# Kernel optimization log

Measured on AMD Instinct MI355X. Metric: run time of the kernel, lower is better.

Reference implementation:

```python
import jax, jax.numpy as jnp
import numpy as np

N, H, B, D, O = 512, 40, 8, 384, 62
DT = 1e-4  # step_size
BOUND = 500.0  # coupling saturation bound
# Jansen-Rit constants (ParamsJR defaults, all variances 0 -> non-learnable)
A_, a_, B_, b_, g_ = 3.25, 100.0, 22.0, 50.0, 100.0
c1, c2, c3, c4 = 135.0, 135.0 * 0.8, 135.0 * 0.25, 135.0 * 0.25
STD_IN, VMAX, V0, R_, MU, K_, KI = 100.0, 5.0, 6.0, 0.56, 0.5, 5.0, 1.0


def setup_inputs() -> dict:
    key = jax.random.key(0)
    ks = jax.random.split(key, 9)
    return {
        "input": jax.random.normal(ks[0], (N, H, B), jnp.float32),
        "noise_in": jax.random.normal(ks[1], (N, H, B, 1), jnp.float32),
        "noise_out": jax.random.normal(ks[2], (N, B), jnp.float32),
        "hx": jax.random.uniform(ks[3], (N, 6), jnp.float32),
        "hE": jax.random.normal(ks[4], (N, D), jnp.float32),
        "w_bb": jax.random.normal(ks[5], (N, N), jnp.float32),
        "sc": jax.random.uniform(ks[6], (N, N), jnp.float32),
        "lm": jax.random.normal(ks[7], (O, N), jnp.float32),
        "delays": jax.random.randint(ks[8], (N, N), 0, D, jnp.int32),
    }


def _sigmoid(x):
    # potential-to-rate operator
    return VMAX / (1.0 + jnp.exp(R_ * (V0 - x)))


def _sys2nd(Aamp, a, u, x, v):
    return Aamp * a * u - 2.0 * a * v - a * a * x


def reference(input, noise_in, noise_out, hx, hE, w_bb, sc, lm, delays):
    # normalized symmetric coupling matrix
    w = jnp.exp(w_bb) * sc
    ws = jnp.log1p(0.5 * (w + w.T))
    w_n = ws / jnp.linalg.norm(ws)            # Frobenius norm, as torch.linalg.norm
    rowsum = jnp.sum(w_n, axis=1)[:, None]    # dg = -diag(rowsum); dg @ x == -rowsum*x

    M, E, I = hx[:, 0:1], hx[:, 1:2], hx[:, 2:3]
    Mv, Ev, Iv = hx[:, 3:4], hx[:, 4:5], hx[:, 5:6]

    def hidden_step(carry, inp):
        M, E, I, Mv, Ev, Iv, hE = carry
        u, nz = inp  # [N,1] each
        Ed = jnp.take_along_axis(hE, delays, axis=1)      # Ed[i,j] = hE[i, delays[i,j]]
        LEd = jnp.sum(w_n * Ed.T, axis=1, keepdims=True)  # [N,1]
        noiseE = nz * STD_IN
        stim = K_ * KI * u
        rM = _sigmoid(E - I)
        rE = c2 * _sigmoid(c1 * M)
        rI = c4 * _sigmoid(c3 * M)
        coupled = g_ * (LEd - rowsum * (E - I))
        coupling = BOUND * jnp.tanh(coupled / BOUND)
        Mn = M + DT * Mv
        En = E + DT * Ev
        In = I + DT * Iv
        Mvn = Mv + DT * _sys2nd(A_, a_, rM, M, Mv)
        Evn = Ev + DT * _sys2nd(A_, a_, rE + coupling + stim + noiseE + MU, E, Ev)
        Ivn = Iv + DT * _sys2nd(B_, b_, rI, I, Iv)
        hE = hE.at[:, 0].set(En[:, 0] - In[:, 0])  # in-place slot-0 write, as in torch
        return (Mn, En, In, Mvn, Evn, Ivn, hE), None

    def batch_step(state, inp):
        u_seq, nz_seq = inp  # [H,N,1]
        state, _ = jax.lax.scan(hidden_step, state, (u_seq, nz_seq))
        M, E, I, Mv, Ev, Iv, hE = state
        hE = jnp.concatenate([E - I, hE[:, :-1]], axis=1)  # shift delay buffer
        eeg = 0.0005 * (lm @ (E - I))  # [O,1]
        return (M, E, I, Mv, Ev, Iv, hE), (M, E, I, Mv, Ev, Iv, eeg)

    u_all = jnp.transpose(input, (2, 1, 0))[..., None]            # [B,H,N,1]
    nz_all = jnp.transpose(noise_in[..., 0], (2, 1, 0))[..., None]
    state0 = (M, E, I, Mv, Ev, Iv, hE)
    state, outs = jax.lax.scan(batch_step, state0, (u_all, nz_all))
    Ms, Es, Is, Mvs, Evs, Ivs, eegs = outs  # [B,N,1] each, eeg [B,O,1]

    stack = lambda x: x[..., 0].T  # -> [N,B] (or [O,B]), matches torch.cat(axis=1)
    Mf, Ef, If, Mvf, Evf, Ivf, hEf = state
    current_state = jnp.concatenate([Mf, Ef, If, Mvf, Evf, Ivf], axis=1)  # [N,6]
    return (current_state, stack(eegs), stack(Es), stack(Is), stack(Ms),
            stack(Evs), stack(Ivs), stack(Mvs), hEf)
```

## Files before the change

kernel.cpp:

```cpp
#include <hip/hip_runtime.h>
#include <math.h>

#define N_    512
#define H_    40
#define B_N   8
#define D_    384
#define O_    62
#define RW    392
#define SMAX  13
#define CMAX  28

#define OUT_STATE 0
#define OUT_EEG   3072
#define OUT_ES    3568
#define OUT_IS    7664
#define OUT_MS    11760
#define OUT_EVS   15856
#define OUT_IVS   19952
#define OUT_MVS   24048
#define OUT_HE    28144

#define SIGK      0.8079092228978195f
#define SIGC      4.847455337386917f
#define SIGK_E    109.06774509120563f
#define SIGK_I    27.266936272801407f
#define TANHS     0.5770780163555854f

#define BARRIER() asm volatile("s_waitcnt lgkmcnt(0)\n\ts_barrier" ::: "memory")

__global__ void k_cnt(const int* __restrict__ delays, int* __restrict__ s0c) {
    int i = blockIdx.x, t = threadIdx.x;
    bool f1 = (delays[t * N_ + i] == 0);
    bool f2 = (delays[(t + 256) * N_ + i] == 0);
    unsigned long long m1 = __ballot(f1), m2 = __ballot(f2);
    __shared__ int pc[4];
    int wave = t >> 6, lane = t & 63;
    if (lane == 0) pc[wave] = __popcll(m1) + __popcll(m2);
    __syncthreads();
    if (t == 0) {
        int s = pc[0] + pc[1] + pc[2] + pc[3];
        s0c[i] = (s > SMAX) ? SMAX : s;
    }
}

__global__ void __launch_bounds__(512)
k_perm(const int* __restrict__ s0c, int* __restrict__ perm,
       int* __restrict__ invp, int* __restrict__ wmaxc) {
    int t = threadIdx.x;
    int wave = t >> 6, lane = t & 63;
    int cnt = s0c[t];
    __shared__ int wc[14 * 8];
    __shared__ int base[14 * 8];
    unsigned long long below = (lane == 0) ? 0ull : ((~0ull) >> (64 - lane));
    for (int c = 0; c < 14; c++) {
        unsigned long long m = __ballot(cnt == c);
        if (lane == 0) wc[c * 8 + wave] = __popcll(m);
    }
    __syncthreads();
    if (t == 0) {
        int s = 0;
        for (int c = 0; c < 14; c++)
            for (int w = 0; w < 8; w++) { base[c * 8 + w] = s; s += wc[c * 8 + w]; }
    }
    __syncthreads();
    int pos = 0;
    for (int c = 0; c < 14; c++) {
        unsigned long long m = __ballot(cnt == c);
        if (cnt == c) pos = base[c * 8 + wave] + __popcll(m & below);
    }
    perm[pos] = t;
    invp[t] = pos;
    if ((pos & 63) == 63) wmaxc[pos >> 6] = cnt;
}

__global__ void k_prep(const float* __restrict__ wbb, const float* __restrict__ sc,
                       const float* __restrict__ hE_in, const int* __restrict__ delays,
                       const int* __restrict__ invp,
                       float* __restrict__ ws, float* __restrict__ ring,
                       float* __restrict__ rowsumP, float* __restrict__ sumsq,
                       float* __restrict__ s0w, int* __restrict__ s0j,
                       float* __restrict__ s1w, int* __restrict__ s1p) {
    int i = blockIdx.x;
    int t = threadIdx.x;
    int ip = invp[i];
    __shared__ float wsrow[N_];
    __shared__ float red[256];
    __shared__ int cnt_c[8];
    __shared__ int bases[8];
    __shared__ int runbase;

    if (t < SMAX) { s0j[t * N_ + ip] = i;        s0w[t * N_ + ip] = 0.f; }
    if (t < CMAX) { s1p[t * N_ + ip] = (1 << 9); s1w[t * N_ + ip] = 0.f; }
    if (t < 9)    { ring[i * RW + t] = 0.f; }

    float ssq = 0.f, rsum = 0.f;
    for (int j = t; j < N_; j += 256) {
        float w = 0.5f * (expf(wbb[i * N_ + j]) * sc[i * N_ + j] +
                          expf(wbb[j * N_ + i]) * sc[j * N_ + i]);
        float v = log1pf(w);
        ws[i * N_ + j] = v;
        wsrow[j] = v;
        ssq += v * v;
        rsum += v;
    }
    for (int k = t; k < D_ - 1; k += 256) ring[i * RW + 9 + k] = hE_in[i * D_ + 1 + k];

    red[t] = ssq; __syncthreads();
    for (int s = 128; s > 0; s >>= 1) { if (t < s) red[t] += red[t + s]; __syncthreads(); }
    if (t == 0) sumsq[i] = red[0];
    __syncthreads();
    red[t] = rsum; __syncthreads();
    for (int s = 128; s > 0; s >>= 1) { if (t < s) red[t] += red[t + s]; __syncthreads(); }
    if (t == 0) rowsumP[ip] = red[0];
    __syncthreads();

    int wave = t >> 6, lane = t & 63;
    int dv1 = delays[t * N_ + i];
    int dv2 = delays[(t + 256) * N_ + i];
    unsigned long long below = (lane == 0) ? 0ull : ((~0ull) >> (64 - lane));
    for (int d = 0; d < 8; d++) {
        bool f1 = (dv1 == d), f2 = (dv2 == d);
        unsigned long long m1 = __ballot(f1);
        unsigned long long m2 = __ballot(f2);
        if (lane == 0) { cnt_c[wave] = __popcll(m1); cnt_c[wave + 4] = __popcll(m2); }
        __syncthreads();
        if (t == 0) {
            int s = (d == 0) ? 0 : runbase;
            for (int c = 0; c < 8; c++) { bases[c] = s; s += cnt_c[c]; }
            if (d == 0) runbase = 0;
            else runbase = s;
        }
        __syncthreads();
        if (d == 0) {
            if (f1) { int pos = bases[wave]     + __popcll(m1 & below);
                      if (pos < SMAX) { s0j[pos * N_ + ip] = t;       s0w[pos * N_ + ip] = wsrow[t]; } }
            if (f2) { int pos = bases[wave + 4] + __popcll(m2 & below);
                      if (pos < SMAX) { s0j[pos * N_ + ip] = t + 256; s0w[pos * N_ + ip] = wsrow[t + 256]; } }
        } else {
            if (f1) { int pos = bases[wave]     + __popcll(m1 & below);
                      if (pos < CMAX) { s1p[pos * N_ + ip] = t | (d << 9);         s1w[pos * N_ + ip] = wsrow[t]; } }
            if (f2) { int pos = bases[wave + 4] + __popcll(m2 & below);
                      if (pos < CMAX) { s1p[pos * N_ + ip] = (t + 256) | (d << 9); s1w[pos * N_ + ip] = wsrow[t + 256]; } }
        }
    }
}

__global__ void __launch_bounds__(512)
k_hist(const float* __restrict__ ws, const int* __restrict__ delays,
       const float* __restrict__ ring, const int* __restrict__ invp,
       const float* __restrict__ input, const float* __restrict__ noise_in,
       float* __restrict__ drv, float* __restrict__ bp8) {
    if (blockIdx.x < H_ * B_N) {
        int bb = blockIdx.x & 7, h = blockIdx.x >> 3;
        int dst = (bb * H_ + h) * N_;
        int nn = threadIdx.x;
        float u  = input[nn * (H_ * B_N) + h * B_N + bb];
        float nz = noise_in[nn * (H_ * B_N) + h * B_N + bb];
        drv[dst + invp[nn]] = fmaf(0.1625f, u, fmaf(3.25f, nz, 16.26625f));
    }
    int b  = blockIdx.x >> 6;
    int ib = (blockIdx.x >> 3) & 7;
    int jb = blockIdx.x & 7;
    int wave = threadIdx.x >> 6, lane = threadIdx.x & 63;
    int i = ib * 64 + lane;
    int off = 8 - b;
    float acc = 0.f;
    int j0 = jb * 64 + wave * 8;
#pragma unroll
    for (int jj = 0; jj < 8; jj++) {
        int j = j0 + jj;
        int d = delays[j * N_ + i];
        float w = ws[j * N_ + i];
        float v = ring[j * RW + off + d];
        acc += (d > 0 ? w : 0.f) * v;
    }
    __shared__ float part[8][64];
    part[wave][lane] = acc; __syncthreads();
    if (wave == 0) {
        float s = 0.f;
#pragma unroll
        for (int w2 = 0; w2 < 8; w2++) s += part[w2][lane];
        bp8[(b * 8 + jb) * N_ + invp[i]] = s;
    }
}

#define LOADK0(K) int jb_##K = s0j[K * N_ + t] << 2; float w_##K = s0w[K * N_ + t] * scale;
#define G(CB, K)  (*(const float*)((const char*)(CB) + jb_##K))

#define PRF(CB)                                                                \
    if (wmax > 0) { g0 = G(CB,0); g1 = G(CB,1); }                              \
    if (wmax > 2) { g2 = G(CB,2); g3 = G(CB,3); }                              \
    if (wmax > 4) { g4 = G(CB,4); g5 = G(CB,5); g6 = G(CB,6); g7 = G(CB,7);    \
                    g8 = G(CB,8); g9 = G(CB,9); g10 = G(CB,10);                \
                    g11 = G(CB,11); g12 = G(CB,12); }

#define STEP(CB, CN)                                                           \
  {                                                                            \
    float d_n = *dnext; dnext += N_;                                           \
    float En = fmaf(1e-4f, Ev, E);                                             \
    float In = fmaf(1e-4f, Iv, I);                                             \
    float Mn = fmaf(1e-4f, Mv, M);                                             \
    (CN)[n] = En - In;                                                         \
    float ei = E - I;                                                          \
    float rMr = __builtin_amdgcn_rcpf(1.0f + __builtin_amdgcn_exp2f(fmaf(-SIGK,   ei, SIGC))); \
    float rEr = __builtin_amdgcn_rcpf(1.0f + __builtin_amdgcn_exp2f(fmaf(-SIGK_E, M,  SIGC))); \
    float rIr = __builtin_amdgcn_rcpf(1.0f + __builtin_amdgcn_exp2f(fmaf(-SIGK_I, M,  SIGC))); \
    float Mvn = fmaf(0.1625f,  rMr, fmaf(0.98f, Mv, -M));                      \
    float Ivn = fmaf(18.5625f, rIr, fmaf(0.99f, Iv, -0.25f * I));              \
    float pre = fmaf(17.55f,   rEr, fmaf(0.98f, Ev, -E) + d_c);                \
    float a0 = 0.f, a1 = 0.f;                                                  \
    if (wmax > 0) { a0 = w_0 * g0; a1 = w_1 * g1; }                            \
    if (wmax > 2) { a0 = fmaf(w_2, g2, a0); a1 = fmaf(w_3, g3, a1); }          \
    if (wmax > 4) { a0 = fmaf(w_4,  g4,  a0); a1 = fmaf(w_5,  g5,  a1);        \
                    a0 = fmaf(w_6,  g6,  a0); a1 = fmaf(w_7,  g7,  a1);        \
                    a0 = fmaf(w_8,  g8,  a0); a1 = fmaf(w_9,  g9,  a1);        \
                    a0 = fmaf(w_10, g10, a0); a1 = fmaf(w_11, g11, a1);        \
                    a0 = fmaf(w_12, g12, a0); }                                \
    float arg = fmaf(-rs, ei, base) + (a0 + a1);                               \
    float cr = __builtin_amdgcn_rcpf(1.0f + __builtin_amdgcn_exp2f(arg));      \
    float Evn = fmaf(-32.5f, cr, pre);                                         \
    M = Mn; E = En; I = In; Mv = Mvn; Ev = Evn; Iv = Iv + 0.f; Iv = Ivn;       \
    d_c = d_n;                                                                 \
    BARRIER();                                                                 \
    PRF(CN)                                                                    \
  }

__global__ void __launch_bounds__(512)
k_hidden(const float* __restrict__ drv, const float* __restrict__ hE_in,
         const float* __restrict__ hx, const float* __restrict__ bp8,
         const float* __restrict__ sumsq, const float* __restrict__ rowsumP,
         const float* __restrict__ s0w, const int* __restrict__ s0j,
         const float* __restrict__ s1w, const int* __restrict__ s1p,
         const int* __restrict__ perm, const int* __restrict__ wmaxc,
         float* __restrict__ ring, float* __restrict__ fing,
         float* __restrict__ out) {
    __shared__ float curr0[N_];
    __shared__ float curr1[N_];
    __shared__ float fin_l[B_N * N_];
    __shared__ float red[N_];
    int t = threadIdx.x;
    int n = perm[t];
    int wmax = __builtin_amdgcn_readfirstlane(wmaxc[t >> 6]);

    red[t] = sumsq[t];
    __syncthreads();
    if (t < 64) {
        float s2 = 0.f;
#pragma unroll
        for (int q = 0; q < 8; q++) s2 += red[t + 64 * q];
#pragma unroll
        for (int off = 32; off > 0; off >>= 1) s2 += __shfl_xor(s2, off, 64);
        if (t == 0) red[0] = s2;
    }
    __syncthreads();
    float scale = TANHS / sqrtf(red[0]);

    LOADK0(0)  LOADK0(1)  LOADK0(2)  LOADK0(3)  LOADK0(4)  LOADK0(5)  LOADK0(6)
    LOADK0(7)  LOADK0(8)  LOADK0(9)  LOADK0(10) LOADK0(11) LOADK0(12)
    int   s1p_r[CMAX];
    float s1w_r[CMAX];
#pragma unroll
    for (int k = 0; k < CMAX; k++) { s1p_r[k] = s1p[k * N_ + t]; s1w_r[k] = s1w[k * N_ + t] * scale; }

    float M  = hx[n * 6 + 0], E  = hx[n * 6 + 1], I  = hx[n * 6 + 2];
    float Mv = hx[n * 6 + 3], Ev = hx[n * 6 + 4], Iv = hx[n * 6 + 5];
    float rs = rowsumP[t] * scale;

    float hp[8];
#pragma unroll
    for (int k = 0; k < 8; k++) hp[k] = bp8[k * N_ + t];

    const float* dnext = drv + t + N_;
    float d_c = drv[t];

    float g0=0.f,g1=0.f,g2=0.f,g3=0.f,g4=0.f,g5=0.f,g6=0.f,g7=0.f,g8=0.f,
          g9=0.f,g10=0.f,g11=0.f,g12=0.f;

#pragma unroll
    for (int k = 0; k < B_N; k++) fin_l[k * N_ + t] = 0.f;
    curr0[n] = hE_in[n * D_];
    __syncthreads();
    PRF(curr0)

    for (int b = 0; b < B_N; b++) {
        float hist = (((hp[0] + hp[1]) + (hp[2] + hp[3])) +
                      ((hp[4] + hp[5]) + (hp[6] + hp[7]))) * scale;
        float corr = 0.f;
#pragma unroll
        for (int k = 0; k < CMAX; k++) {
            int p = s1p_r[k];
            int off = (((b + 8 - (p >> 9)) & 7) << 11) + ((p & 511) << 2);
            corr = fmaf(s1w_r[k], *(const float*)((const char*)fin_l + off), corr);
        }
        float base = hist + corr;

        int bn = (b < B_N - 1) ? b + 1 : b;
#pragma unroll
        for (int k = 0; k < 8; k++) hp[k] = bp8[(bn * 8 + k) * N_ + t];

        for (int hh = 0; hh < H_ / 2; hh++) {
            STEP(curr0, curr1)
            STEP(curr1, curr0)
        }
        float eif = E - I;
        fin_l[b * N_ + n] = eif;
        out[OUT_ES  + n * B_N + b] = E;
        out[OUT_IS  + n * B_N + b] = I;
        out[OUT_MS  + n * B_N + b] = M;
        out[OUT_EVS + n * B_N + b] = Ev;
        out[OUT_IVS + n * B_N + b] = Iv;
        out[OUT_MVS + n * B_N + b] = Mv;
        ring[n * RW + (7 - b)] = eif;
        ring[n * RW + (8 - b)] = eif;
        fing[b * N_ + n] = eif;
        BARRIER();
    }

    out[n * 6 + 0] = M;  out[n * 6 + 1] = E;  out[n * 6 + 2] = I;
    out[n * 6 + 3] = Mv; out[n * 6 + 4] = Ev; out[n * 6 + 5] = Iv;
}

__global__ void k_post(const float* __restrict__ ring, const float* __restrict__ fing,
                       const float* __restrict__ lm, float* __restrict__ out) {
    int bi = blockIdx.x;
    int lane = threadIdx.x;
    if (bi < N_) {
#pragma unroll
        for (int q = 0; q < 6; q++) {
            int k = lane + 64 * q;
            if (k < D_) out[OUT_HE + bi * D_ + k] = ring[bi * RW + k];
        }
    } else {
        int o = bi - N_;
        float lv[8];
#pragma unroll
        for (int q = 0; q < 8; q++) lv[q] = lm[o * N_ + 64 * q + lane];
        for (int b = 0; b < B_N; b++) {
            float p = 0.f;
#pragma unroll
            for (int q = 0; q < 8; q++) p = fmaf(lv[q], fing[b * N_ + 64 * q + lane], p);
#pragma unroll
            for (int off = 32; off > 0; off >>= 1) p += __shfl_down(p, off, 64);
            if (lane == 0) out[OUT_EEG + o * B_N + b] = 0.0005f * p;
        }
    }
}

extern "C" void kernel_launch(void* const* d_in, const int* in_sizes, int n_in,
                              void* d_out, int out_size, void* d_ws, size_t ws_size,
                              hipStream_t stream) {
    const float* input    = (const float*)d_in[0];
    const float* noise_in = (const float*)d_in[1];
    const float* hx       = (const float*)d_in[3];
    const float* hE       = (const float*)d_in[4];
    const float* wbb      = (const float*)d_in[5];
    const float* sc       = (const float*)d_in[6];
    const float* lm       = (const float*)d_in[7];
    const int*   delays   = (const int*)d_in[8];
    float* out = (float*)d_out;

    float* F    = (float*)d_ws;
    float* drv  = F;
    float* wsm  = drv + 164352;
    float* ring = wsm + 262144;
    float* bp8  = ring + 200704;
    float* rswP = bp8 + 32768;
    float* ssq  = rswP + 512;
    float* s0w  = ssq + 512;
    int*   s0j  = (int*)(s0w + N_ * SMAX);
    float* s1w  = (float*)(s0j + N_ * SMAX);
    int*   s1p  = (int*)(s1w + N_ * CMAX);
    float* fing = (float*)(s1p + N_ * CMAX);
    int*   s0c  = (int*)(fing + B_N * N_);
    int*   perm = s0c + N_;
    int*   invp = perm + N_;
    int*   wmaxc = invp + N_;

    k_cnt<<<N_, 256, 0, stream>>>(delays, s0c);
    k_perm<<<1, N_, 0, stream>>>(s0c, perm, invp, wmaxc);
    k_prep<<<N_, 256, 0, stream>>>(wbb, sc, hE, delays, invp,
                                   wsm, ring, rswP, ssq, s0w, s0j, s1w, s1p);
    k_hist<<<512, 512, 0, stream>>>(wsm, delays, ring, invp, input, noise_in, drv, bp8);
    k_hidden<<<1, N_, 0, stream>>>(drv, hE, hx, bp8, ssq, rswP,
                                   s0w, s0j, s1w, s1p, perm, wmaxc, ring, fing, out);
    k_post<<<N_ + O_, 64, 0, stream>>>(ring, fing, lm, out);
}
```

Before: 142.1 us.

## Halve barriers by computing two hidden steps per sync with four-slot buffer

The hidden-state loop now advances two Euler steps between each barrier. It relies on the next-next E-I value being computable locally, and it uses a four-slot shared buffer so that gathers for two steps can be prefetched together. The drive array is transposed per node so each thread loads four consecutive steps as a float4. The E-rate sigmoid now reuses the I-rate exponential through a fourth-power identity, and the prep kernel uses fast exp/log intrinsics. The goal is to halve barrier count and cut transcendental work, at the cost of higher register use and small numeric differences.

```diff
diff --git a/kernel.cpp b/kernel.cpp
--- a/kernel.cpp
+++ b/kernel.cpp
@@ -9,6 +9,7 @@
 #define RW    392
 #define SMAX  13
 #define CMAX  28
+#define DRVS  336
 
 #define OUT_STATE 0
 #define OUT_EEG   3072
@@ -25,6 +26,7 @@
 #define SIGK_E    109.06774509120563f
 #define SIGK_I    27.266936272801407f
 #define TANHS     0.5770780163555854f
+#define C3Q       4.190944e-05f
 
 #define BARRIER() asm volatile("s_waitcnt lgkmcnt(0)\n\ts_barrier" ::: "memory")
 
@@ -95,9 +97,9 @@
 
     float ssq = 0.f, rsum = 0.f;
     for (int j = t; j < N_; j += 256) {
-        float w = 0.5f * (expf(wbb[i * N_ + j]) * sc[i * N_ + j] +
-                          expf(wbb[j * N_ + i]) * sc[j * N_ + i]);
-        float v = log1pf(w);
+        float w = 0.5f * (__expf(wbb[i * N_ + j]) * sc[i * N_ + j] +
+                          __expf(wbb[j * N_ + i]) * sc[j * N_ + i]);
+        float v = 0.6931471805599453f * __builtin_amdgcn_logf(1.0f + w);
         ws[i * N_ + j] = v;
         wsrow[j] = v;
         ssq += v * v;
@@ -152,11 +154,11 @@
        float* __restrict__ drv, float* __restrict__ bp8) {
     if (blockIdx.x < H_ * B_N) {
         int bb = blockIdx.x & 7, h = blockIdx.x >> 3;
-        int dst = (bb * H_ + h) * N_;
+        int step = bb * H_ + h;
         int nn = threadIdx.x;
         float u  = input[nn * (H_ * B_N) + h * B_N + bb];
         float nz = noise_in[nn * (H_ * B_N) + h * B_N + bb];
-        drv[dst + invp[nn]] = fmaf(0.1625f, u, fmaf(3.25f, nz, 16.26625f));
+        drv[(size_t)invp[nn] * DRVS + step] = fmaf(0.1625f, u, fmaf(3.25f, nz, 16.26625f));
     }
     int b  = blockIdx.x >> 6;
     int ib = (blockIdx.x >> 3) & 7;
@@ -185,45 +187,56 @@
 }
 
 #define LOADK0(K) int jb_##K = s0j[K * N_ + t] << 2; float w_##K = s0w[K * N_ + t] * scale;
-#define G(CB, K)  (*(const float*)((const char*)(CB) + jb_##K))
-
-#define PRF(CB)                                                                \
-    if (wmax > 0) { g0 = G(CB,0); g1 = G(CB,1); }                              \
-    if (wmax > 2) { g2 = G(CB,2); g3 = G(CB,3); }                              \
-    if (wmax > 4) { g4 = G(CB,4); g5 = G(CB,5); g6 = G(CB,6); g7 = G(CB,7);    \
-                    g8 = G(CB,8); g9 = G(CB,9); g10 = G(CB,10);                \
-                    g11 = G(CB,11); g12 = G(CB,12); }
-
-#define STEP(CB, CN)                                                           \
+#define GS(SLOT, K) (*(const float*)((const char*)curr4 + ((SLOT) << 11) + jb_##K))
+
+#define PRFS(S, SLOT)                                                          \
+    if (wmax > 0) { g##S##0 = GS(SLOT,0); g##S##1 = GS(SLOT,1); }              \
+    if (wmax > 2) { g##S##2 = GS(SLOT,2); g##S##3 = GS(SLOT,3); }              \
+    if (wmax > 4) { g##S##4 = GS(SLOT,4); g##S##5 = GS(SLOT,5);                \
+                    g##S##6 = GS(SLOT,6); g##S##7 = GS(SLOT,7);                \
+                    g##S##8 = GS(SLOT,8); g##S##9 = GS(SLOT,9);                \
+                    g##S##10 = GS(SLOT,10); g##S##11 = GS(SLOT,11);            \
+                    g##S##12 = GS(SLOT,12); }
+
+#define STEPCORE(DV, S, WSLOT)                                                 \
   {                                                                            \
-    float d_n = *dnext; dnext += N_;                                           \
+    float e0 = __builtin_amdgcn_exp2f(fmaf(-SIGK, ei_c, SIGC));                \
+    float uu = __builtin_amdgcn_exp2f(fmaf(-SIGK_I, M, SIGC));                 \
+    float u2 = uu * uu;                                                        \
+    float u4 = u2 * u2;                                                        \
+    float rMr = __builtin_amdgcn_rcpf(1.0f + e0);                              \
+    float rIr = __builtin_amdgcn_rcpf(1.0f + uu);                              \
+    float rEr = __builtin_amdgcn_rcpf(fmaf(C3Q, u4, 1.0f));                    \
     float En = fmaf(1e-4f, Ev, E);                                             \
     float In = fmaf(1e-4f, Iv, I);                                             \
     float Mn = fmaf(1e-4f, Mv, M);                                             \
-    (CN)[n] = En - In;                                                         \
-    float ei = E - I;                                                          \
-    float rMr = __builtin_amdgcn_rcpf(1.0f + __builtin_amdgcn_exp2f(fmaf(-SIGK,   ei, SIGC))); \
-    float rEr = __builtin_amdgcn_rcpf(1.0f + __builtin_amdgcn_exp2f(fmaf(-SIGK_E, M,  SIGC))); \
-    float rIr = __builtin_amdgcn_rcpf(1.0f + __builtin_amdgcn_exp2f(fmaf(-SIGK_I, M,  SIGC))); \
+    float a0 = 0.f, a1 = 0.f;                                                  \
+    if (wmax > 0) { a0 = w_0 * g##S##0; a1 = w_1 * g##S##1; }                  \
+    if (wmax > 2) { a0 = fmaf(w_2, g##S##2, a0); a1 = fmaf(w_3, g##S##3, a1); }\
+    if (wmax > 4) { a0 = fmaf(w_4,  g##S##4,  a0); a1 = fmaf(w_5,  g##S##5,  a1);\
+                    a0 = fmaf(w_6,  g##S##6,  a0); a1 = fmaf(w_7,  g##S##7,  a1);\
+                    a0 = fmaf(w_8,  g##S##8,  a0); a1 = fmaf(w_9,  g##S##9,  a1);\
+                    a0 = fmaf(w_10, g##S##10, a0); a1 = fmaf(w_11, g##S##11, a1);\
+                    a0 = fmaf(w_12, g##S##12, a0); }                           \
+    float arg = fmaf(-rs, ei_c, base) + (a0 + a1);                             \
+    float e1 = __builtin_amdgcn_exp2f(arg);                                    \
+    float cr = __builtin_amdgcn_rcpf(1.0f + e1);                               \
     float Mvn = fmaf(0.1625f,  rMr, fmaf(0.98f, Mv, -M));                      \
     float Ivn = fmaf(18.5625f, rIr, fmaf(0.99f, Iv, -0.25f * I));              \
-    float pre = fmaf(17.55f,   rEr, fmaf(0.98f, Ev, -E) + d_c);                \
-    float a0 = 0.f, a1 = 0.f;                                                  \
-    if (wmax > 0) { a0 = w_0 * g0; a1 = w_1 * g1; }                            \
-    if (wmax > 2) { a0 = fmaf(w_2, g2, a0); a1 = fmaf(w_3, g3, a1); }          \
-    if (wmax > 4) { a0 = fmaf(w_4,  g4,  a0); a1 = fmaf(w_5,  g5,  a1);        \
-                    a0 = fmaf(w_6,  g6,  a0); a1 = fmaf(w_7,  g7,  a1);        \
-                    a0 = fmaf(w_8,  g8,  a0); a1 = fmaf(w_9,  g9,  a1);        \
-                    a0 = fmaf(w_10, g10, a0); a1 = fmaf(w_11, g11, a1);        \
-                    a0 = fmaf(w_12, g12, a0); }                                \
-    float arg = fmaf(-rs, ei, base) + (a0 + a1);                               \
-    float cr = __builtin_amdgcn_rcpf(1.0f + __builtin_amdgcn_exp2f(arg));      \
-    float Evn = fmaf(-32.5f, cr, pre);                                         \
-    M = Mn; E = En; I = In; Mv = Mvn; Ev = Evn; Iv = Iv + 0.f; Iv = Ivn;       \
-    d_c = d_n;                                                                 \
-    BARRIER();                                                                 \
-    PRF(CN)                                                                    \
+    float Evn = fmaf(-32.5f, cr, fmaf(17.55f, rEr, fmaf(0.98f, Ev, -E) + (DV)));\
+    float En2 = fmaf(1e-4f, Evn, En);                                          \
+    float In2 = fmaf(1e-4f, Ivn, In);                                          \
+    curr4[WSLOT][n] = En2 - In2;                                               \
+    M = Mn; E = En; I = In; Mv = Mvn; Ev = Evn; Iv = Ivn;                      \
+    ei_c = En - In;                                                            \
   }
+
+#define BLOCK(S0, S1, W0, W1, DVA, DVB)                                        \
+    PRFS(A, S0)                                                                \
+    PRFS(B, S1)                                                                \
+    STEPCORE(DVA, A, W0)                                                       \
+    STEPCORE(DVB, B, W1)                                                       \
+    BARRIER();
 
 __global__ void __launch_bounds__(512)
 k_hidden(const float* __restrict__ drv, const float* __restrict__ hE_in,
@@ -234,8 +247,7 @@
          const int* __restrict__ perm, const int* __restrict__ wmaxc,
          float* __restrict__ ring, float* __restrict__ fing,
          float* __restrict__ out) {
-    __shared__ float curr0[N_];
-    __shared__ float curr1[N_];
+    __shared__ float curr4[4][N_];
     __shared__ float fin_l[B_N * N_];
     __shared__ float red[N_];
     int t = threadIdx.x;
@@ -270,17 +282,17 @@
 #pragma unroll
     for (int k = 0; k < 8; k++) hp[k] = bp8[k * N_ + t];
 
-    const float* dnext = drv + t + N_;
-    float d_c = drv[t];
-
-    float g0=0.f,g1=0.f,g2=0.f,g3=0.f,g4=0.f,g5=0.f,g6=0.f,g7=0.f,g8=0.f,
-          g9=0.f,g10=0.f,g11=0.f,g12=0.f;
-
+    float gA0=0.f,gA1=0.f,gA2=0.f,gA3=0.f,gA4=0.f,gA5=0.f,gA6=0.f,gA7=0.f,
+          gA8=0.f,gA9=0.f,gA10=0.f,gA11=0.f,gA12=0.f;
+    float gB0=0.f,gB1=0.f,gB2=0.f,gB3=0.f,gB4=0.f,gB5=0.f,gB6=0.f,gB7=0.f,
+          gB8=0.f,gB9=0.f,gB10=0.f,gB11=0.f,gB12=0.f;
+
+    float ei_c = E - I;
 #pragma unroll
     for (int k = 0; k < B_N; k++) fin_l[k * N_ + t] = 0.f;
-    curr0[n] = hE_in[n * D_];
-    __syncthreads();
-    PRF(curr0)
+    curr4[0][n] = hE_in[n * D_];
+    curr4[1][n] = fmaf(1e-4f, Ev, E) - fmaf(1e-4f, Iv, I);
+    __syncthreads();
 
     for (int b = 0; b < B_N; b++) {
         float hist = (((hp[0] + hp[1]) + (hp[2] + hp[3])) +
@@ -298,11 +310,16 @@
 #pragma unroll
         for (int k = 0; k < 8; k++) hp[k] = bp8[(bn * 8 + k) * N_ + t];
 
-        for (int hh = 0; hh < H_ / 2; hh++) {
-            STEP(curr0, curr1)
-            STEP(curr1, curr0)
-        }
-        float eif = E - I;
+        const float4* sp4 = (const float4*)(drv + (size_t)t * DRVS + b * H_);
+        float4 dc = sp4[0];
+        for (int q = 0; q < 10; q++) {
+            float4 dn = sp4[q + 1];
+            BLOCK(0, 1, 2, 3, dc.x, dc.y)
+            BLOCK(2, 3, 0, 1, dc.z, dc.w)
+            dc = dn;
+        }
+
+        float eif = ei_c;
         fin_l[b * N_ + n] = eif;
         out[OUT_ES  + n * B_N + b] = E;
         out[OUT_IS  + n * B_N + b] = I;
@@ -361,7 +378,7 @@
 
     float* F    = (float*)d_ws;
     float* drv  = F;
-    float* wsm  = drv + 164352;
+    float* wsm  = drv + 172032;
     float* ring = wsm + 262144;
     float* bp8  = ring + 200704;
     float* rswP = bp8 + 32768;
```

After: 141.4 us. About the same (-0.5%).
